# Performance work log

Measured on AMD Instinct MI355X. Metric: run time of the kernel, lower is better.

Reference implementation:

```python
import jax, jax.numpy as jnp
import numpy as np

B, N, DIN, DOUT, T, R, H = 4, 384, 128, 128, 4, 4, 8
DK = DOUT // H
SQRT_DK = float(np.sqrt(DK))


def setup_inputs() -> dict:
    key = jax.random.key(0)
    k = jax.random.split(key, 12)
    node_features = jax.random.normal(k[0], (B, N, DIN), jnp.float32)
    nt = jax.random.uniform(k[1], (B, N, T), dtype=jnp.float32)
    node_types_soft = nt / nt.sum(-1, keepdims=True)  # soft type distribution
    adj_matrix_soft = jax.random.uniform(k[2], (B, N, N), dtype=jnp.float32)
    et = jax.random.uniform(k[3], (B, N, N, R), dtype=jnp.float32)
    edge_types_soft = et / et.sum(-1, keepdims=True)  # soft relation distribution
    s = 0.05  # ~xavier scale for 128x128
    return dict(
        node_features=node_features,
        node_types_soft=node_types_soft,
        adj_matrix_soft=adj_matrix_soft,
        edge_types_soft=edge_types_soft,
        kw=jax.random.normal(k[4], (T, DIN, DOUT), jnp.float32) * s,
        kb=jnp.zeros((T, DOUT), jnp.float32),
        qw=jax.random.normal(k[5], (T, DIN, DOUT), jnp.float32) * s,
        qb=jnp.zeros((T, DOUT), jnp.float32),
        vw=jax.random.normal(k[6], (T, DIN, DOUT), jnp.float32) * s,
        vb=jnp.zeros((T, DOUT), jnp.float32),
        aw=jax.random.normal(k[7], (T, DOUT, DOUT), jnp.float32) * s,
        ab=jnp.zeros((T, DOUT), jnp.float32),
        norm_w=jnp.ones((T, DOUT), jnp.float32),
        norm_b=jnp.zeros((T, DOUT), jnp.float32),
        rel_pri=jnp.ones((R, H), jnp.float32),
        rel_att=jax.random.normal(k[8], (R, H, DK, DK), jnp.float32) * 0.1,
        rel_msg=jax.random.normal(k[9], (R, H, DK, DK), jnp.float32) * 0.1,
        skip=jnp.ones((T,), jnp.float32),
    )


def _forward(node_features, node_types_soft, adj_matrix_soft, edge_types_soft,
             kw, kb, qw, qb, vw, vb, aw, ab, norm_w, norm_b,
             rel_pri, rel_att, rel_msg, skip):
    Bq, Nn, _ = node_features.shape
    nt = node_types_soft
    # per-type Q/K/V projections: [B,N,T,H,DK]
    q = (jnp.einsum('bni,tid->bntd', node_features, qw) + qb).reshape(Bq, Nn, T, H, DK)
    kk = (jnp.einsum('bni,tid->bntd', node_features, kw) + kb).reshape(Bq, Nn, T, H, DK)
    v = (jnp.einsum('bni,tid->bntd', node_features, vw) + vb).reshape(Bq, Nn, T, H, DK)

    res_att = jnp.zeros((Bq, Nn, Nn, H), node_features.dtype)
    res_msg = jnp.zeros((Bq, Nn, Nn, H, DK), node_features.dtype)
    for r in range(R):  # small fixed relation count; types/heads fully vectorized
        kr = jnp.einsum('bjshe,hed->bjshd', kk, rel_att[r])
        vr = jnp.einsum('bjshe,hed->bjshd', v, rel_msg[r])
        # fold target-type mask (applied at node j in the original) into k: [B,N,Tt,Ts,H,DK]
        krt = kr[:, :, None] * nt[:, :, :, None, None, None]
        # P[b,i,j,s,h] = sum_{t,d} q[b,i,t,h,d] * nt[b,j,t] * kr[b,j,s,h,d], scaled
        P = jnp.einsum('bithd,bjtshd->bijsh', q, krt) * (rel_pri[r] / SQRT_DK)
        mask = edge_types_soft[..., r] * adj_matrix_soft  # [B,N,N]
        res_att = res_att + jnp.einsum('bijsh,bis->bijh', P, nt) * mask[..., None]
        res_msg = res_msg + jnp.einsum('bijsh,bis,bjshd->bijhd', P, nt, vr) * mask[..., None, None]

    att_sum = res_att.sum(axis=1, keepdims=True)
    safe = jnp.where(att_sum > 1e-6, att_sum, jnp.ones_like(att_sum))
    attw = (res_att / safe) * (att_sum > 1e-6).astype(res_att.dtype)
    agg = jnp.einsum('btsh,btshd->bthd', attw, res_msg).reshape(Bq, Nn, DOUT)

    trans = jnp.einsum('bnd,tdo->bnto', agg, aw) + ab
    trans = jax.nn.gelu(trans, approximate=False)  # dropout = identity at eval
    alpha = jax.nn.sigmoid(skip)[None, None, :, None]
    # in_dim == out_dim -> identity skip projection
    res = trans * alpha + node_features[:, :, None, :] * (1.0 - alpha)
    mean = res.mean(-1, keepdims=True)
    var = res.var(-1, keepdims=True)
    res = (res - mean) / jnp.sqrt(var + 1e-5) * norm_w + norm_b
    return (res * nt[..., None]).sum(axis=2)  # [B,N,DOUT]


def reference(node_features, node_types_soft, adj_matrix_soft, edge_types_soft,
              kw, kb, qw, qb, vw, vb, aw, ab, norm_w, norm_b,
              rel_pri, rel_att, rel_msg, skip):
    return _forward(node_features, node_types_soft, adj_matrix_soft, edge_types_soft,
                    kw, kb, qw, qb, vw, vb, aw, ab, norm_w, norm_b,
                    rel_pri, rel_att, rel_msg, skip)
```

## Files before the change

kernel.cpp:

```cpp
#include <hip/hip_runtime.h>
#include <math.h>

#define Bq 4
#define Nn 384
#define NB 1536
#define TT 4
#define RR 4
#define HH 8
#define DKk 16
#define APART 12288

typedef __attribute__((ext_vector_type(8))) short short8;
typedef __attribute__((ext_vector_type(4))) float f32x4;

__device__ __forceinline__ unsigned short f2bf(float f) {
  unsigned u = __float_as_uint(f);
  u += 0x7FFFu + ((u >> 16) & 1u);
  return (unsigned short)(u >> 16);
}

__device__ __forceinline__ void ld16(const float* __restrict__ p, float* o) {
  const float4* p4 = reinterpret_cast<const float4*>(p);
  float4 a = p4[0], b = p4[1], c = p4[2], d = p4[3];
  o[0]=a.x; o[1]=a.y; o[2]=a.z; o[3]=a.w;
  o[4]=b.x; o[5]=b.y; o[6]=b.z; o[7]=b.w;
  o[8]=c.x; o[9]=c.y; o[10]=c.z; o[11]=c.w;
  o[12]=d.x; o[13]=d.y; o[14]=d.z; o[15]=d.w;
}

__device__ __forceinline__ void bar_lds() {
  asm volatile("s_waitcnt lgkmcnt(0)" ::: "memory");
  __builtin_amdgcn_s_barrier();
}


__global__ __launch_bounds__(256) void k1a_qkv(
    const float* __restrict__ nf,
    const float* __restrict__ qw, const float* __restrict__ qb,
    const float* __restrict__ kw, const float* __restrict__ kb,
    const float* __restrict__ vw, const float* __restrict__ vb,
    float* __restrict__ q_ws, float* __restrict__ kv_k, float* __restrict__ kv_v)
{
  __shared__ float A_s[32][72];
  __shared__ float W_s[32][132];
  int mt = blockIdx.x, t = blockIdx.y, z = blockIdx.z;
  const float* W    = (z == 0) ? qw : ((z == 1) ? kw : vw);
  const float* bias = (z == 0) ? qb : ((z == 1) ? kb : vb);
  int tid = threadIdx.x;
  int colq = (tid & 31)*4, n8 = (tid >> 5)*8;
  float acc[8][4];
#pragma unroll
  for (int u = 0; u < 8; ++u)
#pragma unroll
    for (int c = 0; c < 4; ++c) acc[u][c] = 0.f;

  for (int kc = 0; kc < 4; ++kc) {
    __syncthreads();
    {
      int kk = tid & 31, nb0 = tid >> 5;
#pragma unroll
      for (int u = 0; u < 8; ++u)
        A_s[kk][nb0 + u*8] = nf[(size_t)(mt*64 + nb0 + u*8)*128 + kc*32 + kk];
#pragma unroll
      for (int u = 0; u < 4; ++u) {
        int idx = u*256 + tid;
        int wk = idx >> 5, c4 = (idx & 31)*4;
        *(float4*)&W_s[wk][c4] = *(const float4*)&W[(size_t)(t*128 + kc*32 + wk)*128 + c4];
      }
    }
    __syncthreads();
#pragma unroll
    for (int k = 0; k < 32; ++k) {
      float4 w4 = *(float4*)&W_s[k][colq];
      float a0[8];
      *(float4*)&a0[0] = *(float4*)&A_s[k][n8];
      *(float4*)&a0[4] = *(float4*)&A_s[k][n8 + 4];
#pragma unroll
      for (int u = 0; u < 8; ++u) {
        acc[u][0] += a0[u]*w4.x; acc[u][1] += a0[u]*w4.y;
        acc[u][2] += a0[u]*w4.z; acc[u][3] += a0[u]*w4.w;
      }
    }
  }
  float4 bv = *(const float4*)&bias[t*128 + colq];
#pragma unroll
  for (int u = 0; u < 8; ++u) {
    int node = mt*64 + n8 + u;
    float4 o;
    o.x = acc[u][0] + bv.x; o.y = acc[u][1] + bv.y;
    o.z = acc[u][2] + bv.z; o.w = acc[u][3] + bv.w;
    if (z == 0) {
      int h = colq >> 4, d = colq & 15;
      *(float4*)&q_ws[((size_t)h*NB + node)*64 + t*16 + d] = o;
    } else {
      float* dst = (z == 1) ? kv_k : kv_v;
      *(float4*)&dst[(size_t)node*512 + t*128 + colq] = o;
    }
  }
}

__global__ __launch_bounds__(256) void k1b_rel(
    const float* __restrict__ kv_k, const float* __restrict__ kv_v,
    const float* __restrict__ rel_att, const float* __restrict__ rel_msg,
    float* __restrict__ kr_ws, float* __restrict__ vr_ws,
    float* __restrict__ agg)
{
  __shared__ float ra_s[4][16][16];
  __shared__ float rm_s[4][16][16];
  __shared__ float k_s[16][4][17];
  __shared__ float v_s[16][4][17];
  int nb = blockIdx.x, h = blockIdx.y;
  int n0 = nb*16;
  int tid = threadIdx.x;
  agg[(size_t)(n0 + (tid >> 4))*128 + h*16 + (tid & 15)] = 0.f;
#pragma unroll
  for (int u0 = 0; u0 < 4; ++u0) {
    int u = u0*256 + tid;
    int r = u >> 8, e = (u >> 4) & 15, d = u & 15;
    ra_s[r][e][d] = rel_att[((size_t)(r*8 + h)*16 + e)*16 + d];
    rm_s[r][e][d] = rel_msg[((size_t)(r*8 + h)*16 + e)*16 + d];
    int nl = u >> 6, s = (u >> 4) & 3, e2 = u & 15;
    k_s[nl][s][e2] = kv_k[(size_t)(n0 + nl)*512 + s*128 + h*16 + e2];
    v_s[nl][s][e2] = kv_v[(size_t)(n0 + nl)*512 + s*128 + h*16 + e2];
  }
  __syncthreads();
  int nl = tid >> 4, dq = tid & 15;
  size_t obase = ((size_t)h*NB + n0 + nl)*256;
#pragma unroll
  for (int r = 0; r < 4; ++r)
#pragma unroll
    for (int s = 0; s < 4; ++s) {
      float aK = 0.f, aV = 0.f;
#pragma unroll
      for (int e = 0; e < 16; ++e) {
        aK += k_s[nl][s][e] * ra_s[r][e][dq];
        aV += v_s[nl][s][e] * rm_s[r][e][dq];
      }
      kr_ws[obase + r*64 + s*16 + dq] = aK;
      vr_ws[obase + r*64 + s*16 + dq] = aV;
    }
}

__global__ __launch_bounds__(256,2) void k2_att(
    const float* __restrict__ nt, const float* __restrict__ adj,
    const float* __restrict__ ets, const float* __restrict__ rel_pri,
    const float* __restrict__ q_ws, const float* __restrict__ kr_ws,
    float* __restrict__ res_att, float* __restrict__ att_part)
{
  __shared__ float q_s[16*68];
  __shared__ float kr_s[32*260];
  __shared__ float ntj_s[32*4];
  __shared__ float nti_s[16*4];
  int bx = blockIdx.x, h = blockIdx.y, b = blockIdx.z;
  int it = bx >> 1, jh = bx & 1;
  int i0 = it*16;
  int tid = threadIdx.x;
  int j_l = tid>>3, ig = (tid>>1)&3, dh = tid&1;
  {
    int i = tid>>4, f = (tid&15)*4;
    float4 qv = *(const float4*)&q_ws[((size_t)(h*NB) + b*Nn + i0 + i)*64 + f];
    *(float4*)&q_s[i*68 + f] = qv;
  }
  if (tid < 64) nti_s[tid] = nt[(size_t)(b*Nn + i0 + (tid>>2))*TT + (tid&3)];
  float crr[4];
#pragma unroll
  for (int r = 0; r < 4; ++r) crr[r] = rel_pri[r*HH+h]*0.25f;

  for (int jc = jh*6; jc < jh*6 + 6; ++jc) {
    __syncthreads();
    {
      int js = tid>>3, gb = tid&7;
      const float* src = &kr_ws[((size_t)(h*NB) + b*Nn + jc*32 + js)*256];
      float* dst = &kr_s[js*260];
#pragma unroll
      for (int gl = 0; gl < 8; ++gl) {
        int g = gl*8 + gb;
        float4 v = *(const float4*)&src[g*4];
        int r = g>>4, s = (g>>2)&3, qd = g&3;
        int gd = (qd>>1)*32 + r*8 + s*2 + (qd&1);
        *(float4*)&dst[gd*4] = v;
      }
      if (tid < 128) ntj_s[tid] = nt[(size_t)(b*Nn + jc*32 + (tid>>2))*TT + (tid&3)];
    }
    __syncthreads();
    int j = jc*32 + j_l;
    float nt0 = ntj_s[j_l*4+0], nt1 = ntj_s[j_l*4+1];
    float nt2 = ntj_s[j_l*4+2], nt3 = ntj_s[j_l*4+3];
    float qn[4][8];
#pragma unroll
    for (int il = 0; il < 4; ++il) {
      int ib = (ig*4 + il)*68 + dh*8;
#pragma unroll
      for (int dp = 0; dp < 8; ++dp)
        qn[il][dp] = q_s[ib+dp]*nt0 + q_s[ib+16+dp]*nt1 + q_s[ib+32+dp]*nt2 + q_s[ib+48+dp]*nt3;
    }
    float mar[4][4];
#pragma unroll
    for (int il = 0; il < 4; ++il) {
      int i = i0 + ig*4 + il;
      float a = adj[((size_t)b*Nn + i)*Nn + j];
      float4 e4 = *(const float4*)&ets[(((size_t)b*Nn + i)*Nn + j)*RR];
      mar[il][0]=e4.x*a; mar[il][1]=e4.y*a; mar[il][2]=e4.z*a; mar[il][3]=e4.w*a;
    }
    float acc[4] = {0.f,0.f,0.f,0.f};
    const float* kbp = &kr_s[j_l*260 + dh*128];
#pragma unroll
    for (int r = 0; r < 4; ++r) {
      float mr0 = mar[0][r]*crr[r], mr1 = mar[1][r]*crr[r];
      float mr2 = mar[2][r]*crr[r], mr3 = mar[3][r]*crr[r];
#pragma unroll
      for (int s = 0; s < 4; ++s) {
        float kk[8];
        *(float4*)&kk[0] = *(const float4*)&kbp[r*32 + s*8];
        *(float4*)&kk[4] = *(const float4*)&kbp[r*32 + s*8 + 4];
        float d0=0,d1=0,d2=0,d3=0;
#pragma unroll
        for (int dp = 0; dp < 8; ++dp) {
          d0 += qn[0][dp]*kk[dp]; d1 += qn[1][dp]*kk[dp];
          d2 += qn[2][dp]*kk[dp]; d3 += qn[3][dp]*kk[dp];
        }
        d0 += __shfl_xor(d0,1); d1 += __shfl_xor(d1,1);
        d2 += __shfl_xor(d2,1); d3 += __shfl_xor(d3,1);
        acc[0] += mr0*nti_s[(ig*4+0)*4+s]*d0;
        acc[1] += mr1*nti_s[(ig*4+1)*4+s]*d1;
        acc[2] += mr2*nti_s[(ig*4+2)*4+s]*d2;
        acc[3] += mr3*nti_s[(ig*4+3)*4+s]*d3;
      }
    }
    if (dh == 0) {
#pragma unroll
      for (int il = 0; il < 4; ++il)
        res_att[((size_t)(b*HH + h)*Nn + i0 + ig*4 + il)*Nn + j] = acc[il];
    }
    float v = acc[0] + acc[1] + acc[2] + acc[3];
    v += __shfl_xor(v, 2);
    v += __shfl_xor(v, 4);
    if ((tid & 7) == 0)
      att_part[(size_t)it*APART + (size_t)(b*HH + h)*Nn + j] = v;
  }
}

__global__ __launch_bounds__(256) void kc_agg(
    const float* __restrict__ nt, const float* __restrict__ adj,
    const float* __restrict__ ets, const float* __restrict__ rel_pri,
    const float* __restrict__ q_ws, const float* __restrict__ kr_ws,
    const float* __restrict__ vr_ws, const float* __restrict__ res_att,
    const float* __restrict__ att_part, float* __restrict__ agg)
{
  __shared__ __align__(16) unsigned short B_lds[4][64*72];
  __shared__ __align__(16) unsigned short vr_lds[64*72];
  __shared__ __align__(16) unsigned short Z_lds[4][16*72];
  __shared__ float ntj_s[256];
  __shared__ float inv_s[64];
  int it = blockIdx.x, jc = blockIdx.y, bh = blockIdx.z;
  int b = bh >> 3, h = bh & 7;
  int tid = threadIdx.x, w = tid >> 6, l = tid & 63;
  int j0 = jc*64;
  int ib = it*64 + w*16;
  int irow = ib + (l & 15);
  int iz = ib + ((l >> 4) << 2);
  int lq = (l >> 4) * 8;
  ntj_s[tid] = nt[(size_t)(b*Nn + j0 + (tid>>2))*4 + (tid&3)];
  if (tid < 64) {
    float s = 0.f;
#pragma unroll
    for (int p = 0; p < 24; ++p)
      s += att_part[(size_t)p*APART + (size_t)bh*Nn + j0 + tid];
    inv_s[tid] = (s > 1e-6f) ? 1.f/s : 0.f;
  }
  short8 af[4][2];
  {
    float q0[8], q1[8];
    const float* qp = &q_ws[((size_t)h*NB + b*Nn + irow)*64];
    *(float4*)&q0[0] = *(const float4*)&qp[lq];
    *(float4*)&q0[4] = *(const float4*)&qp[lq + 4];
    *(float4*)&q1[0] = *(const float4*)&qp[32 + lq];
    *(float4*)&q1[4] = *(const float4*)&qp[32 + lq + 4];
    float4 ntiv = *(const float4*)&nt[(size_t)(b*Nn + irow)*4];
    float nta[4] = {ntiv.x, ntiv.y, ntiv.z, ntiv.w};
#pragma unroll
    for (int s = 0; s < 4; ++s)
#pragma unroll
      for (int e = 0; e < 8; ++e) {
        af[s][0][e] = (short)f2bf(q0[e]*nta[s]);
        af[s][1][e] = (short)f2bf(q1[e]*nta[s]);
      }
  }
  float crv[4];
#pragma unroll
  for (int r = 0; r < 4; ++r) crv[r] = rel_pri[r*HH + h]*0.25f;
  float cw[4][4];
  int eo[4][4];
  const float* ebase = ets + (size_t)b*Nn*Nn*4;
#pragma unroll
  for (int tj = 0; tj < 4; ++tj) {
    int j = j0 + tj*16 + (l & 15);
#pragma unroll
    for (int p = 0; p < 4; ++p) {
      int i = iz + p;
      cw[tj][p] = res_att[((size_t)bh*Nn + i)*Nn + j]
                * adj[((size_t)b*Nn + i)*Nn + j];
      eo[tj][p] = (i*Nn + j)*4;
    }
  }
  f32x4 agg_acc = {0.f,0.f,0.f,0.f};
  int js = tid >> 2, ss = tid & 3;
  const float* krp = &kr_ws[((size_t)h*NB + b*Nn + j0 + js)*256 + ss*16];
  const float* vrp = &vr_ws[((size_t)h*NB + b*Nn + j0 + js)*256 + ss*16];
  float kvA[16], vvA[16];
  ld16(krp, kvA);
  ld16(vrp, vvA);
  bar_lds();
#pragma unroll
  for (int tj = 0; tj < 4; ++tj) {
    float inv = inv_s[tj*16 + (l & 15)];
#pragma unroll
    for (int p = 0; p < 4; ++p) cw[tj][p] *= inv;
  }

#pragma unroll
  for (int r = 0; r < 4; ++r) {
    if (r) bar_lds();
    {
      float crr = crv[r];
      float4 ntjv = *(const float4*)&ntj_s[js*4];
      float nta[4] = {ntjv.x*crr, ntjv.y*crr, ntjv.z*crr, ntjv.w*crr};
#pragma unroll
      for (int t = 0; t < 4; ++t) {
#pragma unroll
        for (int dq = 0; dq < 2; ++dq) {
          short8 v;
#pragma unroll
          for (int e = 0; e < 8; ++e) v[e] = (short)f2bf(kvA[dq*8 + e]*nta[t]);
          *(short8*)&B_lds[ss][js*72 + t*16 + dq*8] = v;
        }
      }
#pragma unroll
      for (int d = 0; d < 16; ++d)
        vr_lds[(ss*16 + d)*72 + js] = f2bf(vvA[d]);
    }
    float kvB[16], vvB[16];
    if (r < 3) {
      ld16(krp + (r+1)*64, kvB);
      ld16(vrp + (r+1)*64, vvB);
    }
    bar_lds();
    float coef[4][4];
#pragma unroll
    for (int tj = 0; tj < 4; ++tj)
#pragma unroll
      for (int p = 0; p < 4; ++p)
        coef[tj][p] = ebase[eo[tj][p] + r] * cw[tj][p];
#pragma unroll
    for (int s = 0; s < 4; ++s) {
      f32x4 wacc[4];
#pragma unroll
      for (int tj = 0; tj < 4; ++tj) wacc[tj] = (f32x4){0.f,0.f,0.f,0.f};
#pragma unroll
      for (int tj = 0; tj < 4; ++tj) {
        short8 b0 = *(const short8*)&B_lds[s][(tj*16 + (l & 15))*72 + lq];
        short8 b1 = *(const short8*)&B_lds[s][(tj*16 + (l & 15))*72 + 32 + lq];
        wacc[tj] = __builtin_amdgcn_mfma_f32_16x16x32_bf16(af[s][0], b0, wacc[tj], 0, 0, 0);
        wacc[tj] = __builtin_amdgcn_mfma_f32_16x16x32_bf16(af[s][1], b1, wacc[tj], 0, 0, 0);
      }
#pragma unroll
      for (int tj = 0; tj < 4; ++tj)
#pragma unroll
        for (int p = 0; p < 4; ++p)
          Z_lds[w][(((l >> 4)*4) + p)*72 + tj*16 + (l & 15)] = f2bf(wacc[tj][p]*coef[tj][p]);
#pragma unroll
      for (int kj = 0; kj < 2; ++kj) {
        short8 zf = *(const short8*)&Z_lds[w][(l & 15)*72 + kj*32 + lq];
        short8 vf = *(const short8*)&vr_lds[(s*16 + (l & 15))*72 + kj*32 + lq];
        agg_acc = __builtin_amdgcn_mfma_f32_16x16x32_bf16(zf, vf, agg_acc, 0, 0, 0);
      }
    }
    if (r < 3) {
#pragma unroll
      for (int e = 0; e < 16; ++e) { kvA[e] = kvB[e]; vvA[e] = vvB[e]; }
    }
  }
#pragma unroll
  for (int p = 0; p < 4; ++p)
    atomicAdd(&agg[((size_t)b*Nn + iz + p)*128 + h*16 + (l & 15)], agg_acc[p]);
}

__global__ __launch_bounds__(128) void k5_out(
    const float* __restrict__ agg_ws, const float* __restrict__ nf,
    const float* __restrict__ nt, const float* __restrict__ aw,
    const float* __restrict__ ab, const float* __restrict__ norm_w,
    const float* __restrict__ norm_b, const float* __restrict__ skip,
    float* __restrict__ out)
{
  __shared__ float agg_s[128];
  __shared__ float red[4];
  int n = blockIdx.x, b = blockIdx.y;
  int o = threadIdx.x;
  size_t node = (size_t)b*Nn + n;
  agg_s[o] = agg_ws[node*128 + o];
  __syncthreads();
  float nfo = nf[node*128 + o];
  float outacc = 0.f;
  for (int t = 0; t < TT; ++t) {
    float a = ab[t*128 + o];
    for (int dd = 0; dd < 128; ++dd) a += agg_s[dd] * aw[(size_t)(t*128 + dd)*128 + o];
    float g = 0.5f * a * (1.f + erff(a * 0.70710678118654752f));
    float alpha = 1.f / (1.f + expf(-skip[t]));
    float res = g*alpha + nfo*(1.f - alpha);
    float s1 = res, s2 = res*res;
#pragma unroll
    for (int m = 32; m >= 1; m >>= 1) { s1 += __shfl_xor(s1, m); s2 += __shfl_xor(s2, m); }
    int w = o >> 6;
    if ((o & 63) == 0) { red[w*2] = s1; red[w*2 + 1] = s2; }
    __syncthreads();
    float tot1 = red[0] + red[2], tot2 = red[1] + red[3];
    __syncthreads();
    float mean = tot1 * (1.f/128.f);
    float var  = tot2 * (1.f/128.f) - mean*mean;
    float nrm = (res - mean) * rsqrtf(var + 1e-5f) * norm_w[t*128 + o] + norm_b[t*128 + o];
    outacc += nrm * nt[node*TT + t];
  }
  out[node*128 + o] = outacc;
}

extern "C" void kernel_launch(void* const* d_in, const int* in_sizes, int n_in,
                              void* d_out, int out_size, void* d_ws, size_t ws_size,
                              hipStream_t stream) {
  const float* nf      = (const float*)d_in[0];
  const float* nts     = (const float*)d_in[1];
  const float* adj     = (const float*)d_in[2];
  const float* ets     = (const float*)d_in[3];
  const float* kw      = (const float*)d_in[4];
  const float* kb      = (const float*)d_in[5];
  const float* qw      = (const float*)d_in[6];
  const float* qb      = (const float*)d_in[7];
  const float* vw      = (const float*)d_in[8];
  const float* vb      = (const float*)d_in[9];
  const float* aw      = (const float*)d_in[10];
  const float* ab      = (const float*)d_in[11];
  const float* normw   = (const float*)d_in[12];
  const float* normb   = (const float*)d_in[13];
  const float* rel_pri = (const float*)d_in[14];
  const float* rel_att = (const float*)d_in[15];
  const float* rel_msg = (const float*)d_in[16];
  const float* skip    = (const float*)d_in[17];
  (void)in_sizes; (void)n_in; (void)out_size; (void)ws_size;

  float* ws = (float*)d_ws;
  float* q_ws    = ws;
  float* kr_ws   = q_ws + 786432;
  float* vr_ws   = kr_ws + 3145728;
  float* res_att = vr_ws + 3145728;
  float* att_part= res_att + 4718592;
  float* agg_ws  = att_part + 294912 + 12288;
  float* kv_k = res_att;
  float* kv_v = res_att + 786432;

  hipLaunchKernelGGL(k1a_qkv, dim3(24, 4, 3), dim3(256), 0, stream,
                     nf, qw, qb, kw, kb, vw, vb, q_ws, kv_k, kv_v);
  hipLaunchKernelGGL(k1b_rel, dim3(96, 8), dim3(256), 0, stream,
                     kv_k, kv_v, rel_att, rel_msg, kr_ws, vr_ws, agg_ws);
  hipLaunchKernelGGL(k2_att, dim3(48, 8, 4), dim3(256), 0, stream,
                     nts, adj, ets, rel_pri, q_ws, kr_ws, res_att, att_part);
  hipLaunchKernelGGL(kc_agg, dim3(6, 6, 32), dim3(256), 0, stream,
                     nts, adj, ets, rel_pri, q_ws, kr_ws, vr_ws, res_att, att_part, agg_ws);
  hipLaunchKernelGGL(k5_out, dim3(384, 4), dim3(128), 0, stream,
                     agg_ws, nf, nts, aw, ab, normw, normb, skip, (float*)d_out);
}
```

Baseline: 194.6 us.

## Double k2_att row tile to 32 rows per block for more K reuse

The attention-score kernel now handles 32 query rows per block instead of 16. Each thread computes 8 rows instead of 4, so every K-relation vector loaded from LDS serves twice as many dot products. The grid is halved and the partial-sum count read in kc_agg drops from 24 to 12 to match. The q tile is stored in a different LDS layout so it can be read with vector loads, and node-type weights are kept in registers instead of LDS. In exchange, register pressure rises under a launch bound of 2 blocks, and fewer blocks are available to fill the GPU.

```diff
diff --git a/kernel.cpp b/kernel.cpp
--- a/kernel.cpp
+++ b/kernel.cpp
@@ -147,21 +147,29 @@
     const float* __restrict__ q_ws, const float* __restrict__ kr_ws,
     float* __restrict__ res_att, float* __restrict__ att_part)
 {
-  __shared__ float q_s[16*68];
+  __shared__ float q_s[32*68];
   __shared__ float kr_s[32*260];
   __shared__ float ntj_s[32*4];
-  __shared__ float nti_s[16*4];
   int bx = blockIdx.x, h = blockIdx.y, b = blockIdx.z;
   int it = bx >> 1, jh = bx & 1;
-  int i0 = it*16;
+  int i0 = it*32;
   int tid = threadIdx.x;
   int j_l = tid>>3, ig = (tid>>1)&3, dh = tid&1;
   {
-    int i = tid>>4, f = (tid&15)*4;
-    float4 qv = *(const float4*)&q_ws[((size_t)(h*NB) + b*Nn + i0 + i)*64 + f];
-    *(float4*)&q_s[i*68 + f] = qv;
-  }
-  if (tid < 64) nti_s[tid] = nt[(size_t)(b*Nn + i0 + (tid>>2))*TT + (tid&3)];
+    int row = tid >> 3, k = tid & 7;
+    const float* src = &q_ws[((size_t)(h*NB) + b*Nn + i0 + row)*64 + k*8];
+    float4 v0 = *(const float4*)&src[0];
+    float4 v1 = *(const float4*)&src[4];
+    int dst = row*68 + (k & 1)*32 + (k >> 1)*8;
+    *(float4*)&q_s[dst] = v0;
+    *(float4*)&q_s[dst + 4] = v1;
+  }
+  float ntiv[8][4];
+#pragma unroll
+  for (int il = 0; il < 8; ++il) {
+    float4 v = *(const float4*)&nt[(size_t)(b*Nn + i0 + il*4 + ig)*TT];
+    ntiv[il][0]=v.x; ntiv[il][1]=v.y; ntiv[il][2]=v.z; ntiv[il][3]=v.w;
+  }
   float crr[4];
 #pragma unroll
   for (int r = 0; r < 4; ++r) crr[r] = rel_pri[r*HH+h]*0.25f;
@@ -186,53 +194,63 @@
     int j = jc*32 + j_l;
     float nt0 = ntj_s[j_l*4+0], nt1 = ntj_s[j_l*4+1];
     float nt2 = ntj_s[j_l*4+2], nt3 = ntj_s[j_l*4+3];
-    float qn[4][8];
-#pragma unroll
-    for (int il = 0; il < 4; ++il) {
-      int ib = (ig*4 + il)*68 + dh*8;
-#pragma unroll
-      for (int dp = 0; dp < 8; ++dp)
-        qn[il][dp] = q_s[ib+dp]*nt0 + q_s[ib+16+dp]*nt1 + q_s[ib+32+dp]*nt2 + q_s[ib+48+dp]*nt3;
-    }
-    float mar[4][4];
-#pragma unroll
-    for (int il = 0; il < 4; ++il) {
-      int i = i0 + ig*4 + il;
+    float qn[8][8];
+#pragma unroll
+    for (int il = 0; il < 8; ++il) {
+      const float* qb2 = &q_s[(il*4 + ig)*68 + dh*32];
+      float4 a0 = *(const float4*)&qb2[0],  a1 = *(const float4*)&qb2[4];
+      float4 b0 = *(const float4*)&qb2[8],  b1 = *(const float4*)&qb2[12];
+      float4 c0 = *(const float4*)&qb2[16], c1 = *(const float4*)&qb2[20];
+      float4 d0 = *(const float4*)&qb2[24], d1 = *(const float4*)&qb2[28];
+      qn[il][0] = a0.x*nt0 + b0.x*nt1 + c0.x*nt2 + d0.x*nt3;
+      qn[il][1] = a0.y*nt0 + b0.y*nt1 + c0.y*nt2 + d0.y*nt3;
+      qn[il][2] = a0.z*nt0 + b0.z*nt1 + c0.z*nt2 + d0.z*nt3;
+      qn[il][3] = a0.w*nt0 + b0.w*nt1 + c0.w*nt2 + d0.w*nt3;
+      qn[il][4] = a1.x*nt0 + b1.x*nt1 + c1.x*nt2 + d1.x*nt3;
+      qn[il][5] = a1.y*nt0 + b1.y*nt1 + c1.y*nt2 + d1.y*nt3;
+      qn[il][6] = a1.z*nt0 + b1.z*nt1 + c1.z*nt2 + d1.z*nt3;
+      qn[il][7] = a1.w*nt0 + b1.w*nt1 + c1.w*nt2 + d1.w*nt3;
+    }
+    float mar[8][4];
+#pragma unroll
+    for (int il = 0; il < 8; ++il) {
+      int i = i0 + il*4 + ig;
       float a = adj[((size_t)b*Nn + i)*Nn + j];
       float4 e4 = *(const float4*)&ets[(((size_t)b*Nn + i)*Nn + j)*RR];
-      mar[il][0]=e4.x*a; mar[il][1]=e4.y*a; mar[il][2]=e4.z*a; mar[il][3]=e4.w*a;
-    }
-    float acc[4] = {0.f,0.f,0.f,0.f};
+      mar[il][0]=e4.x*a*crr[0]; mar[il][1]=e4.y*a*crr[1];
+      mar[il][2]=e4.z*a*crr[2]; mar[il][3]=e4.w*a*crr[3];
+    }
+    float acc[8];
+#pragma unroll
+    for (int il = 0; il < 8; ++il) acc[il] = 0.f;
     const float* kbp = &kr_s[j_l*260 + dh*128];
 #pragma unroll
     for (int r = 0; r < 4; ++r) {
-      float mr0 = mar[0][r]*crr[r], mr1 = mar[1][r]*crr[r];
-      float mr2 = mar[2][r]*crr[r], mr3 = mar[3][r]*crr[r];
 #pragma unroll
       for (int s = 0; s < 4; ++s) {
         float kk[8];
         *(float4*)&kk[0] = *(const float4*)&kbp[r*32 + s*8];
         *(float4*)&kk[4] = *(const float4*)&kbp[r*32 + s*8 + 4];
-        float d0=0,d1=0,d2=0,d3=0;
-#pragma unroll
-        for (int dp = 0; dp < 8; ++dp) {
-          d0 += qn[0][dp]*kk[dp]; d1 += qn[1][dp]*kk[dp];
-          d2 += qn[2][dp]*kk[dp]; d3 += qn[3][dp]*kk[dp];
+        float dd[8];
+#pragma unroll
+        for (int il = 0; il < 8; ++il) {
+          float d0 = qn[il][0]*kk[0] + qn[il][1]*kk[1] + qn[il][2]*kk[2] + qn[il][3]*kk[3]
+                   + qn[il][4]*kk[4] + qn[il][5]*kk[5] + qn[il][6]*kk[6] + qn[il][7]*kk[7];
+          dd[il] = d0;
         }
-        d0 += __shfl_xor(d0,1); d1 += __shfl_xor(d1,1);
-        d2 += __shfl_xor(d2,1); d3 += __shfl_xor(d3,1);
-        acc[0] += mr0*nti_s[(ig*4+0)*4+s]*d0;
-        acc[1] += mr1*nti_s[(ig*4+1)*4+s]*d1;
-        acc[2] += mr2*nti_s[(ig*4+2)*4+s]*d2;
-        acc[3] += mr3*nti_s[(ig*4+3)*4+s]*d3;
+#pragma unroll
+        for (int il = 0; il < 8; ++il) {
+          float dtot = dd[il] + __shfl_xor(dd[il], 1);
+          acc[il] += mar[il][r] * ntiv[il][s] * dtot;
+        }
       }
     }
     if (dh == 0) {
 #pragma unroll
-      for (int il = 0; il < 4; ++il)
-        res_att[((size_t)(b*HH + h)*Nn + i0 + ig*4 + il)*Nn + j] = acc[il];
-    }
-    float v = acc[0] + acc[1] + acc[2] + acc[3];
+      for (int il = 0; il < 8; ++il)
+        res_att[((size_t)(b*HH + h)*Nn + i0 + il*4 + ig)*Nn + j] = acc[il];
+    }
+    float v = acc[0]+acc[1]+acc[2]+acc[3]+acc[4]+acc[5]+acc[6]+acc[7];
     v += __shfl_xor(v, 2);
     v += __shfl_xor(v, 4);
     if ((tid & 7) == 0)
@@ -264,7 +282,7 @@
   if (tid < 64) {
     float s = 0.f;
 #pragma unroll
-    for (int p = 0; p < 24; ++p)
+    for (int p = 0; p < 12; ++p)
       s += att_part[(size_t)p*APART + (size_t)bh*Nn + j0 + tid];
     inv_s[tid] = (s > 1e-6f) ? 1.f/s : 0.f;
   }
@@ -460,7 +478,7 @@
                      nf, qw, qb, kw, kb, vw, vb, q_ws, kv_k, kv_v);
   hipLaunchKernelGGL(k1b_rel, dim3(96, 8), dim3(256), 0, stream,
                      kv_k, kv_v, rel_att, rel_msg, kr_ws, vr_ws, agg_ws);
-  hipLaunchKernelGGL(k2_att, dim3(48, 8, 4), dim3(256), 0, stream,
+  hipLaunchKernelGGL(k2_att, dim3(24, 8, 4), dim3(256), 0, stream,
                      nts, adj, ets, rel_pri, q_ws, kr_ws, res_att, att_part);
   hipLaunchKernelGGL(kc_agg, dim3(6, 6, 32), dim3(256), 0, stream,
                      nts, adj, ets, rel_pri, q_ws, kr_ws, vr_ws, res_att, att_part, agg_ws);
```

Result: slower. 212.3 us (+9.1%).
